# Optimization experiments

Measured on AMD Instinct MI355X. Metric: run time of the kernel, lower is better.

The kernel has to match this reference:

```python
import jax, jax.numpy as jnp
import numpy as np

DIM = 128
N = 32  # hardcoded node count in the original (cnt = zeros(32), d<32 guards)
E = 400000
EPS = 1e-5


def _layernorm(x, g, b):
    m = jnp.mean(x, axis=-1, keepdims=True)
    v = jnp.var(x, axis=-1, keepdims=True)
    return (x - m) / jnp.sqrt(v + EPS) * g + b


def setup_inputs() -> dict:
    key = jax.random.key(0)
    ks = jax.random.split(key, 20)
    s = 0.02
    inp = {
        'nt': jax.random.randint(ks[0], (N,), 0, 20),
        'tr': jax.random.randint(ks[1], (N,), 0, 6),
        'es': jax.random.randint(ks[2], (E,), 0, 32),
        'ed': jax.random.randint(ks[3], (E,), 0, 32),
        'ef': jax.random.randint(ks[4], (E,), 0, 6),
        'ne_w': jax.random.normal(ks[5], (20, DIM), jnp.float32) * s,
        'te_w': jax.random.normal(ks[6], (6, DIM), jnp.float32) * s,
        'ef_w': jax.random.normal(ks[7], (6, DIM), jnp.float32) * s,
        'w_ih': jax.random.normal(ks[8], (3 * DIM, DIM), jnp.float32) * s,
        'w_hh': jax.random.normal(ks[9], (3 * DIM, DIM), jnp.float32) * s,
        'b_ih': jnp.zeros((3 * DIM,), jnp.float32),
        'b_hh': jnp.zeros((3 * DIM,), jnp.float32),
        'ln_g': jnp.ones((DIM,), jnp.float32),
        'ln_b': jnp.zeros((DIM,), jnp.float32),
        'fc1_w': jax.random.normal(ks[10], (DIM, 2 * DIM), jnp.float32) * s,
        'fc1_b': jnp.zeros((DIM,), jnp.float32),
        'ln2_g': jnp.ones((DIM,), jnp.float32),
        'ln2_b': jnp.zeros((DIM,), jnp.float32),
        'fc2_w': jax.random.normal(ks[11], (1, DIM), jnp.float32) * s,
        'fc2_b': jnp.zeros((1,), jnp.float32),
    }
    return inp


def reference(nt, tr, es, ed, ef, ne_w, te_w, ef_w, w_ih, w_hh, b_ih, b_hh,
              ln_g, ln_b, fc1_w, fc1_b, ln2_g, ln2_b, fc2_w, fc2_b):
    h = ne_w[nt] + te_w[tr]            # [N, D]
    edge_feat = ef_w[ef]               # [E, D]

    valid = (ed < N) & (es < N)        # faithful to `if d < 32 and s < 32`
    seg = jnp.where(valid, ed, N)      # invalid edges go to a scratch segment
    src = jnp.minimum(es, N - 1)       # safe gather index (masked below)
    vmask = valid[:, None].astype(h.dtype)

    # degree count is index-only and identical every iteration
    cnt = jax.ops.segment_sum(valid.astype(h.dtype), seg, num_segments=N + 1)[:N]
    cnt = jnp.maximum(cnt, 1.0)[:, None]

    for _ in range(5):
        msg = (h[src] + edge_feat) * vmask                    # [E, D]
        agg = jax.ops.segment_sum(msg, seg, num_segments=N + 1)[:N] / cnt
        # torch GRUCell
        gi = agg @ w_ih.T + b_ih                              # [N, 3D]
        gh = h @ w_hh.T + b_hh
        i_r, i_z, i_n = jnp.split(gi, 3, axis=-1)
        h_r, h_z, h_n = jnp.split(gh, 3, axis=-1)
        r = jax.nn.sigmoid(i_r + h_r)
        z = jax.nn.sigmoid(i_z + h_z)
        n = jnp.tanh(i_n + r * h_n)
        h = _layernorm((1.0 - z) * n + z * h, ln_g, ln_b)

    pooled = jnp.concatenate([h.mean(axis=0), h.max(axis=0)], axis=-1)  # [2D]
    x = pooled @ fc1_w.T + fc1_b
    x = jax.nn.relu(_layernorm(x, ln2_g, ln2_b))              # dropout: eval mode
    out = x @ fc2_w.T + fc2_b                                 # [1]
    return out.squeeze(-1)
```

## Files before the change

kernel.cpp:

```cpp
#include <hip/hip_runtime.h>
#include <math.h>

#define N_NODES 32
#define DIM     128
#define NTHR_H  256
#define HIST_BLOCKS 64
#define NTHR_P  256
#define PACK_BLOCKS 48
#define NTHR_G  512

#define SHS 132
#define SBS 136
#define STS 40

typedef __attribute__((ext_vector_type(8))) short bf16x8;
typedef __attribute__((ext_vector_type(4))) float f32x4;

__device__ __forceinline__ unsigned short f2bf(float f) {
  unsigned int u = __float_as_uint(f);
  u += 0x7fffu + ((u >> 16) & 1u);
  return (unsigned short)(u >> 16);
}

#define LOG2E 1.44269504088896340736f
__device__ __forceinline__ float fexp2(float x) { return __builtin_amdgcn_exp2f(x); }
__device__ __forceinline__ float frcp(float x)  { return __builtin_amdgcn_rcpf(x); }
__device__ __forceinline__ float sigm(float x)  { return frcp(1.f + fexp2(-LOG2E * x)); }
__device__ __forceinline__ float ftanh(float x) { return 1.f - 2.f * frcp(1.f + fexp2((2.f * LOG2E) * x)); }

__global__ __launch_bounds__(NTHR_H) void hist_kernel(
    const int* __restrict__ es, const int* __restrict__ ed,
    const int* __restrict__ ef, int E,
    int* __restrict__ hA, int* __restrict__ hF)
{
  __shared__ int lA[N_NODES * N_NODES];
  __shared__ int lF[N_NODES * 6];
  const int t = threadIdx.x;
  for (int i = t; i < N_NODES * N_NODES; i += NTHR_H) lA[i] = 0;
  for (int i = t; i < N_NODES * 6;       i += NTHR_H) lF[i] = 0;
  __syncthreads();

  const int E4 = E >> 2;
  const int4* es4 = (const int4*)es;
  const int4* ed4 = (const int4*)ed;
  const int4* ef4 = (const int4*)ef;
  #define DO_EDGE(S, D, F) \
    if ((unsigned)(S) < N_NODES && (unsigned)(D) < N_NODES) { \
      atomicAdd(&lA[(D) * N_NODES + (S)], 1); \
      atomicAdd(&lF[(D) * 6 + (F)], 1); }
  for (int i = blockIdx.x * NTHR_H + t; i < E4; i += gridDim.x * NTHR_H) {
    int4 s4 = es4[i], d4 = ed4[i], f4 = ef4[i];
    DO_EDGE(s4.x, d4.x, f4.x)
    DO_EDGE(s4.y, d4.y, f4.y)
    DO_EDGE(s4.z, d4.z, f4.z)
    DO_EDGE(s4.w, d4.w, f4.w)
  }
  if (blockIdx.x == 0) {
    for (int e = (E4 << 2) + t; e < E; e += NTHR_H) {
      int s = es[e], d = ed[e], f = ef[e];
      DO_EDGE(s, d, f)
    }
  }
  #undef DO_EDGE
  __syncthreads();
  for (int i = t; i < N_NODES * N_NODES; i += NTHR_H) { int v = lA[i]; if (v) atomicAdd(&hA[i], v); }
  for (int i = t; i < N_NODES * 6;       i += NTHR_H) { int v = lF[i]; if (v) atomicAdd(&hF[i], v); }
}

__global__ __launch_bounds__(NTHR_P) void pack_kernel(
    const float* __restrict__ w_ih, const float* __restrict__ w_hh,
    unsigned short* __restrict__ pack,
    int* __restrict__ hA, int* __restrict__ hF)
{
  if (blockIdx.x == 0) {
    for (int i = threadIdx.x; i < N_NODES * N_NODES; i += NTHR_P) hA[i] = 0;
    for (int i = threadIdx.x; i < N_NODES * 6;       i += NTHR_P) hF[i] = 0;
  }
  const int gid = blockIdx.x * NTHR_P + threadIdx.x;
  const int T = gid >> 6;
  const int l = gid & 63;
  const int mm = T / 96;
  const int t2 = T % 96;
  const int nt = t2 >> 2;
  const int kt = t2 & 3;
  const int row = nt * 16 + (l & 15);
  const int k   = kt * 32 + (l >> 4) * 8;
  const float* src = (mm ? w_hh : w_ih) + (size_t)row * DIM + k;
  bf16x8 out;
#pragma unroll
  for (int j = 0; j < 8; ++j) out[j] = (short)f2bf(src[j]);
  *(bf16x8*)(pack + (size_t)T * 512 + l * 8) = out;
}

struct GnnParams {
  const int* nt; const int* tr;
  const float* ne_w; const float* te_w; const float* ef_w;
  const float* b_ih; const float* b_hh;
  const float* ln_g; const float* ln_b;
  const float* fc1_w; const float* fc1_b;
  const float* ln2_g; const float* ln2_b;
  const float* fc2_w; const float* fc2_b;
  const int* hA; const int* hF;
  const unsigned short* pack;
  float* out;
};

__global__ __launch_bounds__(NTHR_G, 2) void gnn_kernel(GnnParams p)
{
  const int t  = threadIdx.x;
  const int W  = t >> 6;
  const int l  = t & 63;
  const int g  = l >> 4;
  const int li = l & 15;
  const int d0 = W * 16 + g * 4;

  __shared__ __align__(16) float sh[N_NODES * SHS];
  __shared__ __align__(16) float sBnorm[N_NODES * SHS];
  __shared__ __align__(16) unsigned short hbf  [N_NODES * SBS];
  __shared__ __align__(16) unsigned short aggTT[N_NODES * SBS];
  __shared__ __align__(16) unsigned short hbT  [DIM * STS];
  __shared__ __align__(16) unsigned short anormP[2 * 64 * 8];
  __shared__ __align__(16) float part_s[N_NODES * 8];
  __shared__ __align__(16) float part_q[N_NODES * 8];
  __shared__ float sicnt[N_NODES];
  __shared__ int   snt[N_NODES], str[N_NODES], shF[192];
  __shared__ float pooled[2 * DIM], svals[DIM], red[4];

  bf16x8 Bw[6][4];
#pragma unroll
  for (int q = 0; q < 6; ++q)
#pragma unroll
    for (int kt = 0; kt < 4; ++kt) {
      const int T = (q < 3) ? ((q * 8 + W) * 4 + kt)
                            : (96 + ((q - 3) * 8 + W) * 4 + kt);
      Bw[q][kt] = *(const bf16x8*)(p.pack + (size_t)T * 512 + (size_t)l * 8);
    }

  const f32x4 bir = *(const f32x4*)&p.b_ih[d0];
  const f32x4 biz = *(const f32x4*)&p.b_ih[DIM + d0];
  const f32x4 bin = *(const f32x4*)&p.b_ih[2 * DIM + d0];
  const f32x4 bhr = *(const f32x4*)&p.b_hh[d0];
  const f32x4 bhz = *(const f32x4*)&p.b_hh[DIM + d0];
  const f32x4 bhn = *(const f32x4*)&p.b_hh[2 * DIM + d0];
  const f32x4 lg4 = *(const f32x4*)&p.ln_g[d0];
  const f32x4 lb4 = *(const f32x4*)&p.ln_b[d0];

  if (t < 32) { snt[t] = p.nt[t]; str[t] = p.tr[t]; }
  if (t < 192) shF[t] = p.hF[t];
  if (t < 32) {
    int c = 0;
#pragma unroll
    for (int s = 0; s < 32; ++s) c += p.hA[t * 32 + s];
    sicnt[t] = 1.0f / fmaxf((float)c, 1.0f);
  }
  __syncthreads();

  for (int i = t; i < N_NODES * DIM; i += NTHR_G) {
    const int n = i >> 7, d2 = i & (DIM - 1);
    const float v = p.ne_w[snt[n] * DIM + d2] + p.te_w[str[n] * DIM + d2];
    sh[n * SHS + d2] = v;
    const unsigned short bv = f2bf(v);
    hbf[n * SBS + d2] = bv;
    hbT[d2 * STS + n] = bv;
    float acc = 0.f;
#pragma unroll
    for (int f = 0; f < 6; ++f)
      acc = fmaf((float)shF[n * 6 + f], p.ef_w[f * DIM + d2], acc);
    sBnorm[n * SHS + d2] = acc * sicnt[n];
  }
  if (t < 128) {
    const int mt = t >> 6, ll = t & 63;
    const int m = mt * 16 + (ll & 15);
    const float ic = sicnt[m];
#pragma unroll
    for (int j = 0; j < 8; ++j) {
      const int s = (ll >> 4) * 8 + j;
      anormP[(mt * 64 + ll) * 8 + j] = f2bf((float)p.hA[m * 32 + s] * ic);
    }
  }
  __syncthreads();

  const bf16x8 aN0 = *(const bf16x8*)&anormP[l * 8];
  const bf16x8 aN1 = *(const bf16x8*)&anormP[(64 + l) * 8];
  const f32x4 cB0 = *(const f32x4*)&sBnorm[(li)      * SHS + d0];
  const f32x4 cB1 = *(const f32x4*)&sBnorm[(16 + li) * SHS + d0];
  f32x4 hv0 = *(const f32x4*)&sh[(li)      * SHS + d0];
  f32x4 hv1 = *(const f32x4*)&sh[(16 + li) * SHS + d0];
  const f32x4 fz = {0.f, 0.f, 0.f, 0.f};

  for (int it = 0; it < 5; ++it) {
    {
      const bf16x8 hT = *(const bf16x8*)&hbT[(W * 16 + li) * STS + g * 8];
      const f32x4 dA0 = __builtin_amdgcn_mfma_f32_16x16x32_bf16(hT, aN0, cB0, 0, 0, 0);
      const f32x4 dA1 = __builtin_amdgcn_mfma_f32_16x16x32_bf16(hT, aN1, cB1, 0, 0, 0);
      unsigned long long w0 =
          (unsigned long long)f2bf(dA0[0]) |
          ((unsigned long long)f2bf(dA0[1]) << 16) |
          ((unsigned long long)f2bf(dA0[2]) << 32) |
          ((unsigned long long)f2bf(dA0[3]) << 48);
      unsigned long long w1 =
          (unsigned long long)f2bf(dA1[0]) |
          ((unsigned long long)f2bf(dA1[1]) << 16) |
          ((unsigned long long)f2bf(dA1[2]) << 32) |
          ((unsigned long long)f2bf(dA1[3]) << 48);
      *(unsigned long long*)&aggTT[(li)      * SBS + d0] = w0;
      *(unsigned long long*)&aggTT[(16 + li) * SBS + d0] = w1;
    }
    __syncthreads();

    f32x4 Ai[3][2], Hh[3][2];
#pragma unroll
    for (int q = 0; q < 3; ++q) {
      Ai[q][0] = fz; Ai[q][1] = fz; Hh[q][0] = fz; Hh[q][1] = fz;
    }
#pragma unroll
    for (int kt = 0; kt < 4; ++kt) {
      const int ko = kt * 32 + g * 8;
      const bf16x8 xA0 = *(const bf16x8*)&aggTT[(li)      * SBS + ko];
      const bf16x8 xA1 = *(const bf16x8*)&aggTT[(16 + li) * SBS + ko];
      const bf16x8 xH0 = *(const bf16x8*)&hbf  [(li)      * SBS + ko];
      const bf16x8 xH1 = *(const bf16x8*)&hbf  [(16 + li) * SBS + ko];
#pragma unroll
      for (int q = 0; q < 3; ++q) {
        Ai[q][0] = __builtin_amdgcn_mfma_f32_16x16x32_bf16(Bw[q][kt],     xA0, Ai[q][0], 0, 0, 0);
        Ai[q][1] = __builtin_amdgcn_mfma_f32_16x16x32_bf16(Bw[q][kt],     xA1, Ai[q][1], 0, 0, 0);
        Hh[q][0] = __builtin_amdgcn_mfma_f32_16x16x32_bf16(Bw[3 + q][kt], xH0, Hh[q][0], 0, 0, 0);
        Hh[q][1] = __builtin_amdgcn_mfma_f32_16x16x32_bf16(Bw[3 + q][kt], xH1, Hh[q][1], 0, 0, 0);
      }
    }

    f32x4 hp0, hp1;
#pragma unroll
    for (int j = 0; j < 4; ++j) {
      {
        const float r_ = sigm(Ai[0][0][j] + bir[j] + Hh[0][0][j] + bhr[j]);
        const float z_ = sigm(Ai[1][0][j] + biz[j] + Hh[1][0][j] + bhz[j]);
        const float n_ = ftanh(Ai[2][0][j] + bin[j] + r_ * (Hh[2][0][j] + bhn[j]));
        hp0[j] = (1.f - z_) * n_ + z_ * hv0[j];
      }
      {
        const float r_ = sigm(Ai[0][1][j] + bir[j] + Hh[0][1][j] + bhr[j]);
        const float z_ = sigm(Ai[1][1][j] + biz[j] + Hh[1][1][j] + bhz[j]);
        const float n_ = ftanh(Ai[2][1][j] + bin[j] + r_ * (Hh[2][1][j] + bhn[j]));
        hp1[j] = (1.f - z_) * n_ + z_ * hv1[j];
      }
    }
    {
      float s0 = (hp0[0] + hp0[1]) + (hp0[2] + hp0[3]);
      float q0 = (hp0[0] * hp0[0] + hp0[1] * hp0[1]) + (hp0[2] * hp0[2] + hp0[3] * hp0[3]);
      float s1 = (hp1[0] + hp1[1]) + (hp1[2] + hp1[3]);
      float q1 = (hp1[0] * hp1[0] + hp1[1] * hp1[1]) + (hp1[2] * hp1[2] + hp1[3] * hp1[3]);
      s0 += __shfl_xor(s0, 16); q0 += __shfl_xor(q0, 16);
      s1 += __shfl_xor(s1, 16); q1 += __shfl_xor(q1, 16);
      s0 += __shfl_xor(s0, 32); q0 += __shfl_xor(q0, 32);
      s1 += __shfl_xor(s1, 32); q1 += __shfl_xor(q1, 32);
      if (g == 0) {
        part_s[(li)      * 8 + W] = s0;  part_q[(li)      * 8 + W] = q0;
        part_s[(16 + li) * 8 + W] = s1;  part_q[(16 + li) * 8 + W] = q1;
      }
    }
    __syncthreads();

    #define FIN_NODE(NODE, HP, HV)                                             \
    {                                                                          \
      const f32x4 s0 = *(const f32x4*)&part_s[(NODE) * 8];                     \
      const f32x4 s1 = *(const f32x4*)&part_s[(NODE) * 8 + 4];                 \
      const f32x4 q0 = *(const f32x4*)&part_q[(NODE) * 8];                     \
      const f32x4 q1 = *(const f32x4*)&part_q[(NODE) * 8 + 4];                 \
      const float mean = (((s0[0] + s0[1]) + (s0[2] + s0[3])) +                \
                          ((s1[0] + s1[1]) + (s1[2] + s1[3]))) * (1.0f / DIM); \
      const float var  = (((q0[0] + q0[1]) + (q0[2] + q0[3])) +                \
                          ((q1[0] + q1[1]) + (q1[2] + q1[3]))) * (1.0f / DIM)  \
                         - mean * mean;                                        \
      const float rstd = rsqrtf(var + 1e-5f);                                  \
      _Pragma("unroll")                                                        \
      for (int j = 0; j < 4; ++j)                                              \
        HV[j] = (HP[j] - mean) * rstd * lg4[j] + lb4[j];                       \
      unsigned long long wb =                                                  \
          (unsigned long long)f2bf(HV[0]) |                                    \
          ((unsigned long long)f2bf(HV[1]) << 16) |                            \
          ((unsigned long long)f2bf(HV[2]) << 32) |                            \
          ((unsigned long long)f2bf(HV[3]) << 48);                             \
      *(unsigned long long*)&hbf[(NODE) * SBS + d0] = wb;                      \
      hbT[(d0 + 0) * STS + (NODE)] = (unsigned short)(wb & 0xffff);            \
      hbT[(d0 + 1) * STS + (NODE)] = (unsigned short)((wb >> 16) & 0xffff);    \
      hbT[(d0 + 2) * STS + (NODE)] = (unsigned short)((wb >> 32) & 0xffff);    \
      hbT[(d0 + 3) * STS + (NODE)] = (unsigned short)(wb >> 48);               \
      *(f32x4*)&sh[(NODE) * SHS + d0] = HV;                                    \
    }
    FIN_NODE(li,      hp0, hv0)
    FIN_NODE(16 + li, hp1, hv1)
    #undef FIN_NODE
  }
  __syncthreads();

  if (t < DIM) {
    float s = 0.f, mx = -INFINITY;
#pragma unroll
    for (int n2 = 0; n2 < N_NODES; ++n2) {
      const float v = sh[n2 * SHS + t];
      s += v; mx = fmaxf(mx, v);
    }
    pooled[t]       = s * (1.0f / N_NODES);
    pooled[t + DIM] = mx;
  }
  __syncthreads();

  {
    const int row = t >> 2, part = t & 3;
    const float4* w4f = (const float4*)(p.fc1_w + (size_t)row * 2 * DIM + part * 64);
    const float4* p4  = (const float4*)(pooled + part * 64);
    float acc = 0.f;
#pragma unroll
    for (int k = 0; k < 16; ++k) {
      const float4 wv = w4f[k]; const float4 pv = p4[k];
      acc = fmaf(wv.x, pv.x, acc);
      acc = fmaf(wv.y, pv.y, acc);
      acc = fmaf(wv.z, pv.z, acc);
      acc = fmaf(wv.w, pv.w, acc);
    }
    acc += __shfl_xor(acc, 1);
    acc += __shfl_xor(acc, 2);
    if (part == 0) svals[row] = acc + p.fc1_b[row];
  }
  __syncthreads();

  if (t < DIM) {
    float s = svals[t];
#pragma unroll
    for (int o = 32; o > 0; o >>= 1) s += __shfl_down(s, o, 64);
    if ((t & 63) == 0) red[t >> 6] = s;
  }
  __syncthreads();
  const float mean2 = (red[0] + red[1]) * (1.0f / DIM);
  if (t < DIM) {
    const float dx = svals[t] - mean2;
    float s = dx * dx;
#pragma unroll
    for (int o = 32; o > 0; o >>= 1) s += __shfl_down(s, o, 64);
    if ((t & 63) == 0) red[2 + (t >> 6)] = s;
  }
  __syncthreads();
  const float var2  = (red[2] + red[3]) * (1.0f / DIM);
  const float rstd2 = rsqrtf(var2 + 1e-5f);
  __syncthreads();
  if (t < DIM) {
    float x = (svals[t] - mean2) * rstd2 * p.ln2_g[t] + p.ln2_b[t];
    x = fmaxf(x, 0.f);
    float s = x * p.fc2_w[t];
#pragma unroll
    for (int o = 32; o > 0; o >>= 1) s += __shfl_down(s, o, 64);
    if ((t & 63) == 0) red[t >> 6] = s;
  }
  __syncthreads();
  if (t == 0) p.out[0] = red[0] + red[1] + p.fc2_b[0];
}

extern "C" void kernel_launch(void* const* d_in, const int* in_sizes, int n_in,
                              void* d_out, int out_size, void* d_ws, size_t ws_size,
                              hipStream_t stream)
{
  const int*   nt    = (const int*)d_in[0];
  const int*   tr    = (const int*)d_in[1];
  const int*   es    = (const int*)d_in[2];
  const int*   ed    = (const int*)d_in[3];
  const int*   ef    = (const int*)d_in[4];
  const float* ne_w  = (const float*)d_in[5];
  const float* te_w  = (const float*)d_in[6];
  const float* ef_w  = (const float*)d_in[7];
  const float* w_ih  = (const float*)d_in[8];
  const float* w_hh  = (const float*)d_in[9];
  const float* b_ih  = (const float*)d_in[10];
  const float* b_hh  = (const float*)d_in[11];
  const float* ln_g  = (const float*)d_in[12];
  const float* ln_b  = (const float*)d_in[13];
  const float* fc1_w = (const float*)d_in[14];
  const float* fc1_b = (const float*)d_in[15];
  const float* ln2_g = (const float*)d_in[16];
  const float* ln2_b = (const float*)d_in[17];
  const float* fc2_w = (const float*)d_in[18];
  const float* fc2_b = (const float*)d_in[19];

  const int E = in_sizes[2];

  int*            hA   = (int*)d_ws;
  int*            hF   = (int*)((char*)d_ws + 4096);
  unsigned short* pack = (unsigned short*)((char*)d_ws + 8192);

  hipLaunchKernelGGL(pack_kernel, dim3(PACK_BLOCKS), dim3(NTHR_P), 0, stream,
                     w_ih, w_hh, pack, hA, hF);
  hipLaunchKernelGGL(hist_kernel, dim3(HIST_BLOCKS), dim3(NTHR_H), 0, stream,
                     es, ed, ef, E, hA, hF);

  GnnParams prm;
  prm.nt = nt; prm.tr = tr;
  prm.ne_w = ne_w; prm.te_w = te_w; prm.ef_w = ef_w;
  prm.b_ih = b_ih; prm.b_hh = b_hh;
  prm.ln_g = ln_g; prm.ln_b = ln_b;
  prm.fc1_w = fc1_w; prm.fc1_b = fc1_b;
  prm.ln2_g = ln2_g; prm.ln2_b = ln2_b;
  prm.fc2_w = fc2_w; prm.fc2_b = fc2_b;
  prm.hA = hA; prm.hF = hF; prm.pack = pack;
  prm.out = (float*)d_out;

  hipLaunchKernelGGL(gnn_kernel, dim3(1), dim3(NTHR_G), 0, stream, prm);
}
```

Before: 37.52 us.

## Prepack fc1 weights to bf16 and prefetch tail-stage parameters into registers

The pack kernel gains 16 extra blocks that convert fc1_w to bf16 in the workspace. The GNN kernel preloads those into registers at kernel start, along with fc1_b, ln2 and fc2 parameters and the adjacency histogram (staged through shared memory). This takes global loads off the serial single-block tail. The fp32 h store to shared memory now happens only on the last iteration, and the histogram kernel's grid is doubled. The cost is more register pressure, plus lower precision for fc1 weights.

```diff
diff --git a/kernel.cpp b/kernel.cpp
--- a/kernel.cpp
+++ b/kernel.cpp
@@ -4,9 +4,9 @@
 #define N_NODES 32
 #define DIM     128
 #define NTHR_H  256
-#define HIST_BLOCKS 64
+#define HIST_BLOCKS 128
 #define NTHR_P  256
-#define PACK_BLOCKS 48
+#define PACK_BLOCKS 64
 #define NTHR_G  512
 
 #define SHS 132
@@ -20,6 +20,9 @@
   unsigned int u = __float_as_uint(f);
   u += 0x7fffu + ((u >> 16) & 1u);
   return (unsigned short)(u >> 16);
+}
+__device__ __forceinline__ float bf2f(unsigned short b) {
+  return __uint_as_float(((unsigned int)b) << 16);
 }
 
 #define LOG2E 1.44269504088896340736f
@@ -69,27 +72,40 @@
 
 __global__ __launch_bounds__(NTHR_P) void pack_kernel(
     const float* __restrict__ w_ih, const float* __restrict__ w_hh,
-    unsigned short* __restrict__ pack,
+    const float* __restrict__ fc1_w,
+    unsigned short* __restrict__ pack, unsigned short* __restrict__ packF1,
     int* __restrict__ hA, int* __restrict__ hF)
 {
   if (blockIdx.x == 0) {
     for (int i = threadIdx.x; i < N_NODES * N_NODES; i += NTHR_P) hA[i] = 0;
     for (int i = threadIdx.x; i < N_NODES * 6;       i += NTHR_P) hF[i] = 0;
   }
-  const int gid = blockIdx.x * NTHR_P + threadIdx.x;
-  const int T = gid >> 6;
-  const int l = gid & 63;
-  const int mm = T / 96;
-  const int t2 = T % 96;
-  const int nt = t2 >> 2;
-  const int kt = t2 & 3;
-  const int row = nt * 16 + (l & 15);
-  const int k   = kt * 32 + (l >> 4) * 8;
-  const float* src = (mm ? w_hh : w_ih) + (size_t)row * DIM + k;
-  bf16x8 out;
-#pragma unroll
-  for (int j = 0; j < 8; ++j) out[j] = (short)f2bf(src[j]);
-  *(bf16x8*)(pack + (size_t)T * 512 + l * 8) = out;
+  if (blockIdx.x < 48) {
+    const int gid = blockIdx.x * NTHR_P + threadIdx.x;
+    const int T = gid >> 6;
+    const int l = gid & 63;
+    const int mm = T / 96;
+    const int t2 = T % 96;
+    const int nt = t2 >> 2;
+    const int kt = t2 & 3;
+    const int row = nt * 16 + (l & 15);
+    const int k   = kt * 32 + (l >> 4) * 8;
+    const float* src = (mm ? w_hh : w_ih) + (size_t)row * DIM + k;
+    bf16x8 out;
+#pragma unroll
+    for (int j = 0; j < 8; ++j) out[j] = (short)f2bf(src[j]);
+    *(bf16x8*)(pack + (size_t)T * 512 + l * 8) = out;
+  } else {
+    const int j = ((blockIdx.x - 48) * NTHR_P + threadIdx.x) * 8;
+    const float4 lo = *(const float4*)(fc1_w + j);
+    const float4 hi = *(const float4*)(fc1_w + j + 4);
+    bf16x8 v;
+    v[0] = (short)f2bf(lo.x); v[1] = (short)f2bf(lo.y);
+    v[2] = (short)f2bf(lo.z); v[3] = (short)f2bf(lo.w);
+    v[4] = (short)f2bf(hi.x); v[5] = (short)f2bf(hi.y);
+    v[6] = (short)f2bf(hi.z); v[7] = (short)f2bf(hi.w);
+    *(bf16x8*)(packF1 + j) = v;
+  }
 }
 
 struct GnnParams {
@@ -97,11 +113,11 @@
   const float* ne_w; const float* te_w; const float* ef_w;
   const float* b_ih; const float* b_hh;
   const float* ln_g; const float* ln_b;
-  const float* fc1_w; const float* fc1_b;
+  const float* fc1_b;
   const float* ln2_g; const float* ln2_b;
   const float* fc2_w; const float* fc2_b;
   const int* hA; const int* hF;
-  const unsigned short* pack;
+  const unsigned short* pack; const unsigned short* packF1;
   float* out;
 };
 
@@ -122,6 +138,7 @@
   __shared__ __align__(16) unsigned short anormP[2 * 64 * 8];
   __shared__ __align__(16) float part_s[N_NODES * 8];
   __shared__ __align__(16) float part_q[N_NODES * 8];
+  __shared__ __align__(16) int   sAraw[N_NODES * N_NODES];
   __shared__ float sicnt[N_NODES];
   __shared__ int   snt[N_NODES], str[N_NODES], shF[192];
   __shared__ float pooled[2 * DIM], svals[DIM], red[4];
@@ -135,6 +152,10 @@
                             : (96 + ((q - 3) * 8 + W) * 4 + kt);
       Bw[q][kt] = *(const bf16x8*)(p.pack + (size_t)T * 512 + (size_t)l * 8);
     }
+  bf16x8 F1[8];
+#pragma unroll
+  for (int j = 0; j < 8; ++j)
+    F1[j] = *(const bf16x8*)(p.packF1 + (size_t)t * 64 + j * 8);
 
   const f32x4 bir = *(const f32x4*)&p.b_ih[d0];
   const f32x4 biz = *(const f32x4*)&p.b_ih[DIM + d0];
@@ -144,13 +165,21 @@
   const f32x4 bhn = *(const f32x4*)&p.b_hh[2 * DIM + d0];
   const f32x4 lg4 = *(const f32x4*)&p.ln_g[d0];
   const f32x4 lb4 = *(const f32x4*)&p.ln_b[d0];
+  const int2  hAv = *(const int2*)(p.hA + t * 2);
+  const float fc1b_ = p.fc1_b[t >> 2];
+  const float fc2b  = p.fc2_b[0];
+  float ln2g_ = 0.f, ln2b_ = 0.f, f2w_ = 0.f;
+  if (t < DIM) { ln2g_ = p.ln2_g[t]; ln2b_ = p.ln2_b[t]; f2w_ = p.fc2_w[t]; }
 
   if (t < 32) { snt[t] = p.nt[t]; str[t] = p.tr[t]; }
   if (t < 192) shF[t] = p.hF[t];
+  *(int2*)&sAraw[t * 2] = hAv;
+  __syncthreads();
+
   if (t < 32) {
     int c = 0;
 #pragma unroll
-    for (int s = 0; s < 32; ++s) c += p.hA[t * 32 + s];
+    for (int s = 0; s < 32; ++s) c += sAraw[t * 32 + s];
     sicnt[t] = 1.0f / fmaxf((float)c, 1.0f);
   }
   __syncthreads();
@@ -175,7 +204,7 @@
 #pragma unroll
     for (int j = 0; j < 8; ++j) {
       const int s = (ll >> 4) * 8 + j;
-      anormP[(mt * 64 + ll) * 8 + j] = f2bf((float)p.hA[m * 32 + s] * ic);
+      anormP[(mt * 64 + ll) * 8 + j] = f2bf((float)sAraw[m * 32 + s] * ic);
     }
   }
   __syncthreads();
@@ -286,7 +315,7 @@
       hbT[(d0 + 1) * STS + (NODE)] = (unsigned short)((wb >> 16) & 0xffff);    \
       hbT[(d0 + 2) * STS + (NODE)] = (unsigned short)((wb >> 32) & 0xffff);    \
       hbT[(d0 + 3) * STS + (NODE)] = (unsigned short)(wb >> 48);               \
-      *(f32x4*)&sh[(NODE) * SHS + d0] = HV;                                    \
+      if (it == 4) *(f32x4*)&sh[(NODE) * SHS + d0] = HV;                       \
     }
     FIN_NODE(li,      hp0, hv0)
     FIN_NODE(16 + li, hp1, hv1)
@@ -307,21 +336,18 @@
   __syncthreads();
 
   {
-    const int row = t >> 2, part = t & 3;
-    const float4* w4f = (const float4*)(p.fc1_w + (size_t)row * 2 * DIM + part * 64);
-    const float4* p4  = (const float4*)(pooled + part * 64);
+    const int part = t & 3;
     float acc = 0.f;
 #pragma unroll
-    for (int k = 0; k < 16; ++k) {
-      const float4 wv = w4f[k]; const float4 pv = p4[k];
-      acc = fmaf(wv.x, pv.x, acc);
-      acc = fmaf(wv.y, pv.y, acc);
-      acc = fmaf(wv.z, pv.z, acc);
-      acc = fmaf(wv.w, pv.w, acc);
-    }
-    acc += __shfl_xor(acc, 1);
-    acc += __shfl_xor(acc, 2);
-    if (part == 0) svals[row] = acc + p.fc1_b[row];
+    for (int j = 0; j < 8; ++j) {
+      const bf16x8 f = F1[j];
+#pragma unroll
+      for (int e = 0; e < 8; ++e)
+        acc = fmaf(bf2f((unsigned short)f[e]), pooled[part * 64 + j * 8 + e], acc);
+    }
+    acc += __shfl_xor(acc, 1, 4);
+    acc += __shfl_xor(acc, 2, 4);
+    if (part == 0) svals[t >> 2] = acc + fc1b_;
   }
   __syncthreads();
 
@@ -345,15 +371,15 @@
   const float rstd2 = rsqrtf(var2 + 1e-5f);
   __syncthreads();
   if (t < DIM) {
-    float x = (svals[t] - mean2) * rstd2 * p.ln2_g[t] + p.ln2_b[t];
+    float x = (svals[t] - mean2) * rstd2 * ln2g_ + ln2b_;
     x = fmaxf(x, 0.f);
-    float s = x * p.fc2_w[t];
+    float s = x * f2w_;
 #pragma unroll
     for (int o = 32; o > 0; o >>= 1) s += __shfl_down(s, o, 64);
     if ((t & 63) == 0) red[t >> 6] = s;
   }
   __syncthreads();
-  if (t == 0) p.out[0] = red[0] + red[1] + p.fc2_b[0];
+  if (t == 0) p.out[0] = red[0] + red[1] + fc2b;
 }
 
 extern "C" void kernel_launch(void* const* d_in, const int* in_sizes, int n_in,
@@ -383,12 +409,13 @@
 
   const int E = in_sizes[2];
 
-  int*            hA   = (int*)d_ws;
-  int*            hF   = (int*)((char*)d_ws + 4096);
-  unsigned short* pack = (unsigned short*)((char*)d_ws + 8192);
+  int*            hA     = (int*)d_ws;
+  int*            hF     = (int*)((char*)d_ws + 4096);
+  unsigned short* pack   = (unsigned short*)((char*)d_ws + 8192);
+  unsigned short* packF1 = (unsigned short*)((char*)d_ws + 204800);
 
   hipLaunchKernelGGL(pack_kernel, dim3(PACK_BLOCKS), dim3(NTHR_P), 0, stream,
-                     w_ih, w_hh, pack, hA, hF);
+                     w_ih, w_hh, fc1_w, pack, packF1, hA, hF);
   hipLaunchKernelGGL(hist_kernel, dim3(HIST_BLOCKS), dim3(NTHR_H), 0, stream,
                      es, ed, ef, E, hA, hF);
 
@@ -397,10 +424,10 @@
   prm.ne_w = ne_w; prm.te_w = te_w; prm.ef_w = ef_w;
   prm.b_ih = b_ih; prm.b_hh = b_hh;
   prm.ln_g = ln_g; prm.ln_b = ln_b;
-  prm.fc1_w = fc1_w; prm.fc1_b = fc1_b;
+  prm.fc1_b = fc1_b;
   prm.ln2_g = ln2_g; prm.ln2_b = ln2_b;
   prm.fc2_w = fc2_w; prm.fc2_b = fc2_b;
-  prm.hA = hA; prm.hF = hF; prm.pack = pack;
+  prm.hA = hA; prm.hF = hF; prm.pack = pack; prm.packF1 = packF1;
   prm.out = (float*)d_out;
 
   hipLaunchKernelGGL(gnn_kernel, dim3(1), dim3(NTHR_G), 0, stream, prm);
```

After: 40.85 us. +8.8%, slower.

## Fuse histogram, weight packing and GNN into one kernel with flag sync

Applied to the files above, without the earlier changes.

Merges the three separate launches (weight pack, edge histogram, single-block GNN) into one persistent mega-kernel. Block 0 runs the GNN, blocks 1-64 build the histogram and the remaining blocks pack the weights, coordinated through global atomic counters with acquire/release spin-waits. Block 0 overlaps its embedding setup with the producers and only waits before it needs the packed weights or the histograms. The workspace is zeroed with a memset instead of inside the pack kernel. This removes inter-kernel launch gaps, but relies on all blocks being co-resident and adds a memset node plus spin-wait overhead.

```diff
diff --git a/kernel.cpp b/kernel.cpp
--- a/kernel.cpp
+++ b/kernel.cpp
@@ -3,11 +3,10 @@
 
 #define N_NODES 32
 #define DIM     128
-#define NTHR_H  256
-#define HIST_BLOCKS 64
-#define NTHR_P  256
-#define PACK_BLOCKS 48
-#define NTHR_G  512
+#define NTHR    512
+#define HIST_NBLK 64
+#define PACK_NBLK 24
+#define NBLK_TOTAL (1 + HIST_NBLK + PACK_NBLK)
 
 #define SHS 132
 #define SBS 136
@@ -28,71 +27,37 @@
 __device__ __forceinline__ float sigm(float x)  { return frcp(1.f + fexp2(-LOG2E * x)); }
 __device__ __forceinline__ float ftanh(float x) { return 1.f - 2.f * frcp(1.f + fexp2((2.f * LOG2E) * x)); }
 
-__global__ __launch_bounds__(NTHR_H) void hist_kernel(
-    const int* __restrict__ es, const int* __restrict__ ed,
-    const int* __restrict__ ef, int E,
-    int* __restrict__ hA, int* __restrict__ hF)
-{
-  __shared__ int lA[N_NODES * N_NODES];
-  __shared__ int lF[N_NODES * 6];
-  const int t = threadIdx.x;
-  for (int i = t; i < N_NODES * N_NODES; i += NTHR_H) lA[i] = 0;
-  for (int i = t; i < N_NODES * 6;       i += NTHR_H) lF[i] = 0;
-  __syncthreads();
-
-  const int E4 = E >> 2;
-  const int4* es4 = (const int4*)es;
-  const int4* ed4 = (const int4*)ed;
-  const int4* ef4 = (const int4*)ef;
-  #define DO_EDGE(S, D, F) \
-    if ((unsigned)(S) < N_NODES && (unsigned)(D) < N_NODES) { \
-      atomicAdd(&lA[(D) * N_NODES + (S)], 1); \
-      atomicAdd(&lF[(D) * 6 + (F)], 1); }
-  for (int i = blockIdx.x * NTHR_H + t; i < E4; i += gridDim.x * NTHR_H) {
-    int4 s4 = es4[i], d4 = ed4[i], f4 = ef4[i];
-    DO_EDGE(s4.x, d4.x, f4.x)
-    DO_EDGE(s4.y, d4.y, f4.y)
-    DO_EDGE(s4.z, d4.z, f4.z)
-    DO_EDGE(s4.w, d4.w, f4.w)
-  }
-  if (blockIdx.x == 0) {
-    for (int e = (E4 << 2) + t; e < E; e += NTHR_H) {
-      int s = es[e], d = ed[e], f = ef[e];
-      DO_EDGE(s, d, f)
-    }
-  }
-  #undef DO_EDGE
-  __syncthreads();
-  for (int i = t; i < N_NODES * N_NODES; i += NTHR_H) { int v = lA[i]; if (v) atomicAdd(&hA[i], v); }
-  for (int i = t; i < N_NODES * 6;       i += NTHR_H) { int v = lF[i]; if (v) atomicAdd(&hF[i], v); }
-}
-
-__global__ __launch_bounds__(NTHR_P) void pack_kernel(
-    const float* __restrict__ w_ih, const float* __restrict__ w_hh,
-    unsigned short* __restrict__ pack,
-    int* __restrict__ hA, int* __restrict__ hF)
-{
-  if (blockIdx.x == 0) {
-    for (int i = threadIdx.x; i < N_NODES * N_NODES; i += NTHR_P) hA[i] = 0;
-    for (int i = threadIdx.x; i < N_NODES * 6;       i += NTHR_P) hF[i] = 0;
-  }
-  const int gid = blockIdx.x * NTHR_P + threadIdx.x;
-  const int T = gid >> 6;
-  const int l = gid & 63;
-  const int mm = T / 96;
-  const int t2 = T % 96;
-  const int nt = t2 >> 2;
-  const int kt = t2 & 3;
-  const int row = nt * 16 + (l & 15);
-  const int k   = kt * 32 + (l >> 4) * 8;
-  const float* src = (mm ? w_hh : w_ih) + (size_t)row * DIM + k;
-  bf16x8 out;
-#pragma unroll
-  for (int j = 0; j < 8; ++j) out[j] = (short)f2bf(src[j]);
-  *(bf16x8*)(pack + (size_t)T * 512 + l * 8) = out;
-}
-
-struct GnnParams {
+__device__ __forceinline__ void st8_sc1(unsigned long long* p, unsigned long long v) {
+  __hip_atomic_store(p, v, __ATOMIC_RELAXED, __HIP_MEMORY_SCOPE_AGENT);
+}
+__device__ __forceinline__ unsigned long long ld8_sc1(const unsigned long long* p) {
+  return __hip_atomic_load(p, __ATOMIC_RELAXED, __HIP_MEMORY_SCOPE_AGENT);
+}
+__device__ __forceinline__ int ld4_sc1(const int* p) {
+  return __hip_atomic_load(p, __ATOMIC_RELAXED, __HIP_MEMORY_SCOPE_AGENT);
+}
+__device__ __forceinline__ void wait_flag(const int* f, int target) {
+  if (threadIdx.x == 0) {
+    while (__hip_atomic_load(f, __ATOMIC_ACQUIRE, __HIP_MEMORY_SCOPE_AGENT) != target)
+      __builtin_amdgcn_s_sleep(1);
+  }
+  __syncthreads();
+}
+__device__ __forceinline__ void bump_flag(int* f) {
+  __syncthreads();
+  if (threadIdx.x == 0)
+    __hip_atomic_fetch_add(f, 1, __ATOMIC_RELEASE, __HIP_MEMORY_SCOPE_AGENT);
+}
+__device__ __forceinline__ bf16x8 ld_frag_sc1(const unsigned short* pp) {
+  union { unsigned long long u[2]; bf16x8 v; } x;
+  x.u[0] = ld8_sc1((const unsigned long long*)pp);
+  x.u[1] = ld8_sc1((const unsigned long long*)(pp + 4));
+  return x.v;
+}
+
+struct MegaParams {
+  const int* es; const int* ed; const int* ef; int E;
+  const float* w_ih; const float* w_hh;
   const int* nt; const int* tr;
   const float* ne_w; const float* te_w; const float* ef_w;
   const float* b_ih; const float* b_hh;
@@ -100,14 +65,74 @@
   const float* fc1_w; const float* fc1_b;
   const float* ln2_g; const float* ln2_b;
   const float* fc2_w; const float* fc2_b;
-  const int* hA; const int* hF;
-  const unsigned short* pack;
+  int* hA; int* hF; int* flags;
+  unsigned short* pack;
   float* out;
 };
 
-__global__ __launch_bounds__(NTHR_G, 2) void gnn_kernel(GnnParams p)
+__global__ __launch_bounds__(NTHR, 2) void mega_kernel(MegaParams p)
 {
-  const int t  = threadIdx.x;
+  const int b = blockIdx.x;
+  const int t = threadIdx.x;
+
+  if (b >= 1 && b <= HIST_NBLK) {
+    __shared__ int lA[N_NODES * N_NODES];
+    __shared__ int lF[N_NODES * 6];
+    for (int i = t; i < N_NODES * N_NODES; i += NTHR) lA[i] = 0;
+    for (int i = t; i < N_NODES * 6;       i += NTHR) lF[i] = 0;
+    __syncthreads();
+
+    const int b2 = b - 1;
+    const int E4 = p.E >> 2;
+    const int4* es4 = (const int4*)p.es;
+    const int4* ed4 = (const int4*)p.ed;
+    const int4* ef4 = (const int4*)p.ef;
+    #define DO_EDGE(S, D, F) \
+      if ((unsigned)(S) < N_NODES && (unsigned)(D) < N_NODES) { \
+        atomicAdd(&lA[(D) * N_NODES + (S)], 1); \
+        atomicAdd(&lF[(D) * 6 + (F)], 1); }
+    for (int i = b2 * NTHR + t; i < E4; i += HIST_NBLK * NTHR) {
+      int4 s4 = es4[i], d4 = ed4[i], f4 = ef4[i];
+      DO_EDGE(s4.x, d4.x, f4.x)
+      DO_EDGE(s4.y, d4.y, f4.y)
+      DO_EDGE(s4.z, d4.z, f4.z)
+      DO_EDGE(s4.w, d4.w, f4.w)
+    }
+    if (b2 == 0) {
+      for (int e = (E4 << 2) + t; e < p.E; e += NTHR) {
+        int s = p.es[e], d = p.ed[e], f = p.ef[e];
+        DO_EDGE(s, d, f)
+      }
+    }
+    #undef DO_EDGE
+    __syncthreads();
+    for (int i = t; i < N_NODES * N_NODES; i += NTHR) { int v = lA[i]; if (v) atomicAdd(&p.hA[i], v); }
+    for (int i = t; i < N_NODES * 6;       i += NTHR) { int v = lF[i]; if (v) atomicAdd(&p.hF[i], v); }
+    bump_flag(&p.flags[0]);
+    return;
+  }
+
+  if (b > HIST_NBLK) {
+    const int gid = (b - HIST_NBLK - 1) * NTHR + t;
+    const int T = gid >> 6;
+    const int l = gid & 63;
+    const int mm = T / 96;
+    const int t2 = T % 96;
+    const int nt2 = t2 >> 2;
+    const int kt = t2 & 3;
+    const int row = nt2 * 16 + (l & 15);
+    const int k   = kt * 32 + (l >> 4) * 8;
+    const float* src = (mm ? p.w_hh : p.w_ih) + (size_t)row * DIM + k;
+    union { unsigned long long u[2]; unsigned short s[8]; } out;
+#pragma unroll
+    for (int j = 0; j < 8; ++j) out.s[j] = f2bf(src[j]);
+    unsigned long long* dst = (unsigned long long*)(p.pack + (size_t)T * 512 + l * 8);
+    st8_sc1(dst,     out.u[0]);
+    st8_sc1(dst + 1, out.u[1]);
+    bump_flag(&p.flags[1]);
+    return;
+  }
+
   const int W  = t >> 6;
   const int l  = t & 63;
   const int g  = l >> 4;
@@ -122,19 +147,10 @@
   __shared__ __align__(16) unsigned short anormP[2 * 64 * 8];
   __shared__ __align__(16) float part_s[N_NODES * 8];
   __shared__ __align__(16) float part_q[N_NODES * 8];
+  __shared__ __align__(16) int   sAraw[N_NODES * N_NODES];
   __shared__ float sicnt[N_NODES];
   __shared__ int   snt[N_NODES], str[N_NODES], shF[192];
   __shared__ float pooled[2 * DIM], svals[DIM], red[4];
-
-  bf16x8 Bw[6][4];
-#pragma unroll
-  for (int q = 0; q < 6; ++q)
-#pragma unroll
-    for (int kt = 0; kt < 4; ++kt) {
-      const int T = (q < 3) ? ((q * 8 + W) * 4 + kt)
-                            : (96 + ((q - 3) * 8 + W) * 4 + kt);
-      Bw[q][kt] = *(const bf16x8*)(p.pack + (size_t)T * 512 + (size_t)l * 8);
-    }
 
   const f32x4 bir = *(const f32x4*)&p.b_ih[d0];
   const f32x4 biz = *(const f32x4*)&p.b_ih[DIM + d0];
@@ -146,22 +162,46 @@
   const f32x4 lb4 = *(const f32x4*)&p.ln_b[d0];
 
   if (t < 32) { snt[t] = p.nt[t]; str[t] = p.tr[t]; }
-  if (t < 192) shF[t] = p.hF[t];
-  if (t < 32) {
-    int c = 0;
-#pragma unroll
-    for (int s = 0; s < 32; ++s) c += p.hA[t * 32 + s];
-    sicnt[t] = 1.0f / fmaxf((float)c, 1.0f);
-  }
-  __syncthreads();
-
-  for (int i = t; i < N_NODES * DIM; i += NTHR_G) {
+  __syncthreads();
+
+  for (int i = t; i < N_NODES * DIM; i += NTHR) {
     const int n = i >> 7, d2 = i & (DIM - 1);
     const float v = p.ne_w[snt[n] * DIM + d2] + p.te_w[str[n] * DIM + d2];
     sh[n * SHS + d2] = v;
     const unsigned short bv = f2bf(v);
     hbf[n * SBS + d2] = bv;
     hbT[d2 * STS + n] = bv;
+  }
+
+  wait_flag(&p.flags[1], PACK_NBLK);
+  bf16x8 Bw[6][4];
+#pragma unroll
+  for (int q = 0; q < 6; ++q)
+#pragma unroll
+    for (int kt = 0; kt < 4; ++kt) {
+      const int T = (q < 3) ? ((q * 8 + W) * 4 + kt)
+                            : (96 + ((q - 3) * 8 + W) * 4 + kt);
+      Bw[q][kt] = ld_frag_sc1(p.pack + (size_t)T * 512 + (size_t)l * 8);
+    }
+
+  wait_flag(&p.flags[0], HIST_NBLK);
+  {
+    const unsigned long long v = ld8_sc1((const unsigned long long*)p.hA + t);
+    *(unsigned long long*)&sAraw[t * 2] = v;
+  }
+  if (t < 192) shF[t] = ld4_sc1(&p.hF[t]);
+  __syncthreads();
+
+  if (t < 32) {
+    int c = 0;
+#pragma unroll
+    for (int s = 0; s < 32; ++s) c += sAraw[t * 32 + s];
+    sicnt[t] = 1.0f / fmaxf((float)c, 1.0f);
+  }
+  __syncthreads();
+
+  for (int i = t; i < N_NODES * DIM; i += NTHR) {
+    const int n = i >> 7, d2 = i & (DIM - 1);
     float acc = 0.f;
 #pragma unroll
     for (int f = 0; f < 6; ++f)
@@ -175,7 +215,7 @@
 #pragma unroll
     for (int j = 0; j < 8; ++j) {
       const int s = (ll >> 4) * 8 + j;
-      anormP[(mt * 64 + ll) * 8 + j] = f2bf((float)p.hA[m * 32 + s] * ic);
+      anormP[(mt * 64 + ll) * 8 + j] = f2bf((float)sAraw[m * 32 + s] * ic);
     }
   }
   __syncthreads();
@@ -383,25 +423,25 @@
 
   const int E = in_sizes[2];
 
-  int*            hA   = (int*)d_ws;
-  int*            hF   = (int*)((char*)d_ws + 4096);
-  unsigned short* pack = (unsigned short*)((char*)d_ws + 8192);
-
-  hipLaunchKernelGGL(pack_kernel, dim3(PACK_BLOCKS), dim3(NTHR_P), 0, stream,
-                     w_ih, w_hh, pack, hA, hF);
-  hipLaunchKernelGGL(hist_kernel, dim3(HIST_BLOCKS), dim3(NTHR_H), 0, stream,
-                     es, ed, ef, E, hA, hF);
-
-  GnnParams prm;
-  prm.nt = nt; prm.tr = tr;
-  prm.ne_w = ne_w; prm.te_w = te_w; prm.ef_w = ef_w;
-  prm.b_ih = b_ih; prm.b_hh = b_hh;
-  prm.ln_g = ln_g; prm.ln_b = ln_b;
-  prm.fc1_w = fc1_w; prm.fc1_b = fc1_b;
-  prm.ln2_g = ln2_g; prm.ln2_b = ln2_b;
-  prm.fc2_w = fc2_w; prm.fc2_b = fc2_b;
-  prm.hA = hA; prm.hF = hF; prm.pack = pack;
-  prm.out = (float*)d_out;
-
-  hipLaunchKernelGGL(gnn_kernel, dim3(1), dim3(NTHR_G), 0, stream, prm);
-}
+  int*            hA    = (int*)d_ws;
+  int*            hF    = (int*)((char*)d_ws + 4096);
+  int*            flags = (int*)((char*)d_ws + 4992);
+  unsigned short* pack  = (unsigned short*)((char*)d_ws + 8192);
+
+  hipMemsetAsync(d_ws, 0, 5120, stream);
+
+  MegaParams mp;
+  mp.es = es; mp.ed = ed; mp.ef = ef; mp.E = E;
+  mp.w_ih = w_ih; mp.w_hh = w_hh;
+  mp.nt = nt; mp.tr = tr;
+  mp.ne_w = ne_w; mp.te_w = te_w; mp.ef_w = ef_w;
+  mp.b_ih = b_ih; mp.b_hh = b_hh;
+  mp.ln_g = ln_g; mp.ln_b = ln_b;
+  mp.fc1_w = fc1_w; mp.fc1_b = fc1_b;
+  mp.ln2_g = ln2_g; mp.ln2_b = ln2_b;
+  mp.fc2_w = fc2_w; mp.fc2_b = fc2_b;
+  mp.hA = hA; mp.hF = hF; mp.flags = flags; mp.pack = pack;
+  mp.out = (float*)d_out;
+
+  hipLaunchKernelGGL(mega_kernel, dim3(NBLK_TOTAL), dim3(NTHR), 0, stream, mp);
+}
```

New measurement: 36.35 us. -3.1%, faster.
